# Kernel tuning notes

Hardware: AMD Instinct MI355X
Metric: run time of the kernel (lower is better)

The kernel has to match this reference:

```python
import jax, jax.numpy as jnp
import numpy as np


def _conv1d(x, w, pad):
    # torch F.conv1d is cross-correlation; so is lax.conv_general_dilated.
    # x: (k, c_in, N), w: (c_out, c_in, K) -> (k, c_out, N + 2*pad - K + 1)
    return jax.lax.conv_general_dilated(
        x, w, window_strides=(1,), padding=[(pad, pad)],
        dimension_numbers=("NCH", "OIH", "NCH"))


def setup_inputs() -> dict:
    key = jax.random.key(0)
    k1, k2, k3, k4, k5 = jax.random.split(key, 5)
    k_b, c_out, c_in, N, m = 4, 64, 8, 4096, 8
    z_real = jax.random.normal(k1, (k_b, c_in, N), dtype=jnp.float32)
    z_imag = jax.random.normal(k2, (k_b, c_in, N), dtype=jnp.float32)
    A = jax.random.uniform(k3, (c_out, c_in, 1), jnp.float32, 0.75, 1.25)
    beta = jax.random.uniform(k4, (c_out, c_in, 1), jnp.float32, -np.pi, np.pi)
    bias = jax.random.uniform(k5, (c_out, 1), jnp.float32, -0.1, 0.1)
    return {"z_real": z_real, "z_imag": z_imag, "A": A, "beta": beta,
            "bias": bias, "m": m}


def reference(z_real, z_imag, A, beta, bias, m):
    k_b, c_in, N = z_real.shape
    am = abs(int(m))
    ker = N // (2 * am)  # self.ker_size

    # Complex harmonic kernel: |A| * exp(i*(beta + 2*pi*m*phi/N))
    phi = jnp.arange(ker, dtype=jnp.float32)
    ang = beta + (2.0 * jnp.pi * m / N) * phi  # (c_out, c_in, ker)
    absA = jnp.abs(A)
    wr = absA * jnp.cos(ang)
    wi = absA * jnp.sin(ang)

    # Complex conv via 4 real convs: (zr + i zi) * (wr + i wi)
    rr = _conv1d(z_real, wr, ker)
    ii = _conv1d(z_imag, wi, ker)
    ri = _conv1d(z_real, wi, ker)
    ir = _conv1d(z_imag, wr, ker)
    zraw_r = rr - ii  # (k, c_out, N + ker + 1)
    zraw_i = ri + ir

    # Aliasing fold: gather shifted copies, mask out-of-range, alternate sign.
    n = jnp.arange(-2 * am + 1, 2 * am + 1, dtype=jnp.int32)  # (4|m|,)
    mu = jnp.arange(N, dtype=jnp.int32)[:, None]              # (N, 1)
    ind = mu + ker * n                                        # (N, 4|m|)
    cond = ((ind > 0) & (ind < N + ker)).astype(jnp.float32)
    ind = jnp.clip(ind, 0, N + ker)
    menos_1 = (-1.0) ** (1.0 + n.astype(jnp.float32))         # alternating sign
    sign = cond * menos_1                                     # (N, 4|m|)

    gr = zraw_r[:, :, ind]  # (k, c_out, N, 4|m|)
    gi = zraw_i[:, :, ind]
    sr = jnp.einsum("kcnm,nm->kcn", gr, sign)
    si = jnp.einsum("kcnm,nm->kcn", gi, sign)

    # activation: sigmoid(|z| + bias) * z / (|z| + 1e-5)
    mag = jnp.sqrt(sr * sr + si * si)
    gate = jax.nn.sigmoid(mag + bias) / (mag + 1e-5)
    return gate * sr, gate * si
```

## Files before the change

kernel.cpp:

```cpp
#include <hip/hip_runtime.h>
#include <math.h>


#define KB   4
#define COUT 64
#define CIN  8
#define NN   4096
#define INV_N (1.0f / 4096.0f)
#define INV_2PI 0.15915494309189535f

__global__ void f_reduce_kernel(const float* __restrict__ zr,
                                const float* __restrict__ zi,
                                const int* __restrict__ m_ptr,
                                float* __restrict__ F) {
    const int pair = blockIdx.x;
    const int tid  = threadIdx.x;
    const int m    = *m_ptr;
    const float4* xr = (const float4*)(zr + pair * NN);
    const float4* xi = (const float4*)(zi + pair * NN);

    float fcr = 0.f, fsr = 0.f, fci = 0.f, fsi = 0.f;
    #pragma unroll
    for (int it = 0; it < NN / 1024; ++it) {
        int vidx = it * 256 + tid;
        float4 vr = xr[vidx];
        float4 vi = xi[vidx];
        int t0 = vidx * 4;
        #pragma unroll
        for (int j = 0; j < 4; ++j) {
            int r = (m * (t0 + j)) & (NN - 1);
            float rev = (float)r * INV_N;
            float s = __builtin_amdgcn_sinf(rev);
            float c = __builtin_amdgcn_cosf(rev);
            float a = (&vr.x)[j], b = (&vi.x)[j];
            fcr += a * c;  fsr += a * s;
            fci += b * c;  fsi += b * s;
        }
    }
    #pragma unroll
    for (int off = 32; off > 0; off >>= 1) {
        fcr += __shfl_down(fcr, off);
        fsr += __shfl_down(fsr, off);
        fci += __shfl_down(fci, off);
        fsi += __shfl_down(fsi, off);
    }
    __shared__ float red[4][4];
    int wave = tid >> 6, lane = tid & 63;
    if (lane == 0) {
        red[wave][0] = fcr; red[wave][1] = fsr;
        red[wave][2] = fci; red[wave][3] = fsi;
    }
    __syncthreads();
    if (tid == 0) {
        F[pair * 4 + 0] = red[0][0] + red[1][0] + red[2][0] + red[3][0];
        F[pair * 4 + 1] = red[0][1] + red[1][1] + red[2][1] + red[3][1];
        F[pair * 4 + 2] = red[0][2] + red[1][2] + red[2][2] + red[3][2];
        F[pair * 4 + 3] = red[0][3] + red[1][3] + red[2][3] + red[3][3];
    }
}

__global__ void out_kernel(const float* __restrict__ A,
                           const float* __restrict__ beta,
                           const float* __restrict__ bias,
                           const int* __restrict__ m_ptr,
                           const float* __restrict__ F,
                           float* __restrict__ out) {
    const int blk = blockIdx.x;
    const int b = blk >> 6, o = blk & (COUT - 1);
    const int m = *m_ptr;

    float Gr = 0.f, Hr = 0.f, Gi = 0.f, Hi = 0.f;
    #pragma unroll
    for (int i = 0; i < CIN; ++i) {
        float a  = fabsf(A[o * CIN + i]);
        float rb = beta[o * CIN + i] * INV_2PI;
        float sb = __builtin_amdgcn_sinf(rb);
        float cb = __builtin_amdgcn_cosf(rb);
        float P = a * cb, Q = a * sb;
        const float* f = F + (b * CIN + i) * 4;
        float Fcr = f[0], Fsr = f[1], Fci = f[2], Fsi = f[3];
        Gr += -P * Fcr + Q * Fsr + Q * Fci + P * Fsi;
        Hr += -P * Fsr - Q * Fcr + Q * Fsi - P * Fci;
        Gi += -Q * Fcr - P * Fsr - P * Fci + Q * Fsi;
        Hi +=  P * Fcr - Q * Fsr - Q * Fci - P * Fsi;
    }
    const float bo = bias[o];
    const int base = blk << 12;
    const int half = KB * COUT * NN;

    #pragma unroll
    for (int k = 0; k < NN / 256; ++k) {
        int mu = threadIdx.x + k * 256;
        int r = (m * mu) & (NN - 1);
        float rev = (float)r * INV_N;
        float smu = __builtin_amdgcn_sinf(rev);
        float cmu = __builtin_amdgcn_cosf(rev);
        float sr = -(cmu * Gr + smu * Hr);
        float si = -(cmu * Gi + smu * Hi);
        float mag = sqrtf(sr * sr + si * si);
        float gate = 1.0f / (1.0f + __expf(-(mag + bo))) / (mag + 1e-5f);
        out[base + mu]        = gate * sr;
        out[half + base + mu] = gate * si;
    }
}

extern "C" void kernel_launch(void* const* d_in, const int* in_sizes, int n_in,
                              void* d_out, int out_size, void* d_ws, size_t ws_size,
                              hipStream_t stream) {
    const float* z_real = (const float*)d_in[0];
    const float* z_imag = (const float*)d_in[1];
    const float* A      = (const float*)d_in[2];
    const float* beta   = (const float*)d_in[3];
    const float* bias   = (const float*)d_in[4];
    const int*   m_ptr  = (const int*)d_in[5];
    float* out = (float*)d_out;
    float* F   = (float*)d_ws;

    f_reduce_kernel<<<KB * CIN, 256, 0, stream>>>(z_real, z_imag, m_ptr, F);
    out_kernel<<<KB * COUT, 256, 0, stream>>>(A, beta, bias, m_ptr, F, out);
}
```

Measured before the change: 71.17 us.

## Fuse Fourier reduction and output into one kernel per (batch, out-channel)

Merges the two kernels into a single launch. Each block now recomputes the channel-weighted projection of the input against the m-th harmonic directly, then uses the reduced pair to produce its output row. The output stores are vectorised to float4 and the imaginary part is derived from the same two sums. This removes the second launch and the workspace round trip. In exchange each block re-reads the full 8-channel input for its batch, 64 times redundantly overall, and does more trig and FMA work.

Measured after the change: 77.98 us. +9.6%, slower.

```diff
diff --git a/kernel.cpp b/kernel.cpp
--- a/kernel.cpp
+++ b/kernel.cpp
@@ -6,101 +6,101 @@
 #define COUT 64
 #define CIN  8
 #define NN   4096
-#define INV_N (1.0f / 4096.0f)
+#define INV_N   (1.0f / 4096.0f)
 #define INV_2PI 0.15915494309189535f
 
-__global__ void f_reduce_kernel(const float* __restrict__ zr,
-                                const float* __restrict__ zi,
-                                const int* __restrict__ m_ptr,
-                                float* __restrict__ F) {
-    const int pair = blockIdx.x;
-    const int tid  = threadIdx.x;
-    const int m    = *m_ptr;
-    const float4* xr = (const float4*)(zr + pair * NN);
-    const float4* xi = (const float4*)(zi + pair * NN);
+__global__ __launch_bounds__(256) void capa_fused_kernel(
+    const float* __restrict__ zr,
+    const float* __restrict__ zi,
+    const float* __restrict__ A,
+    const float* __restrict__ beta,
+    const float* __restrict__ bias,
+    const int*   __restrict__ m_ptr,
+    float* __restrict__ out) {
 
-    float fcr = 0.f, fsr = 0.f, fci = 0.f, fsi = 0.f;
+    const int blk = blockIdx.x;
+    const int b = blk >> 6, o = blk & (COUT - 1);
+    const int m = *m_ptr;
+    const int tid = threadIdx.x;
+
+    float P[CIN], Q[CIN];
     #pragma unroll
-    for (int it = 0; it < NN / 1024; ++it) {
-        int vidx = it * 256 + tid;
-        float4 vr = xr[vidx];
-        float4 vi = xi[vidx];
+    for (int i = 0; i < CIN; ++i) {
+        float a  = fabsf(A[o * CIN + i]);
+        float rb = beta[o * CIN + i] * INV_2PI;
+        P[i] = a * __builtin_amdgcn_cosf(rb);
+        Q[i] = a * __builtin_amdgcn_sinf(rb);
+    }
+
+    const float4* xr = (const float4*)(zr + b * CIN * NN);
+    const float4* xi = (const float4*)(zi + b * CIN * NN);
+
+    float gr = 0.f, hr = 0.f;
+    #pragma unroll
+    for (int k = 0; k < NN / 4 / 256; ++k) {
+        int vidx = tid + k * 256;
+        float4 vr[CIN], vi[CIN];
+        #pragma unroll
+        for (int i = 0; i < CIN; ++i) {
+            vr[i] = xr[i * (NN / 4) + vidx];
+            vi[i] = xi[i * (NN / 4) + vidx];
+        }
         int t0 = vidx * 4;
         #pragma unroll
         for (int j = 0; j < 4; ++j) {
+            float X = 0.f, Y = 0.f;
+            #pragma unroll
+            for (int i = 0; i < CIN; ++i) {
+                float a = (&vr[i].x)[j];
+                float c2 = (&vi[i].x)[j];
+                X += -P[i] * a + Q[i] * c2;
+                Y +=  Q[i] * a + P[i] * c2;
+            }
             int r = (m * (t0 + j)) & (NN - 1);
             float rev = (float)r * INV_N;
             float s = __builtin_amdgcn_sinf(rev);
             float c = __builtin_amdgcn_cosf(rev);
-            float a = (&vr.x)[j], b = (&vi.x)[j];
-            fcr += a * c;  fsr += a * s;
-            fci += b * c;  fsi += b * s;
+            gr += c * X + s * Y;
+            hr += s * X - c * Y;
         }
     }
+
     #pragma unroll
     for (int off = 32; off > 0; off >>= 1) {
-        fcr += __shfl_down(fcr, off);
-        fsr += __shfl_down(fsr, off);
-        fci += __shfl_down(fci, off);
-        fsi += __shfl_down(fsi, off);
+        gr += __shfl_down(gr, off);
+        hr += __shfl_down(hr, off);
     }
-    __shared__ float red[4][4];
+    __shared__ float red[4][2];
     int wave = tid >> 6, lane = tid & 63;
-    if (lane == 0) {
-        red[wave][0] = fcr; red[wave][1] = fsr;
-        red[wave][2] = fci; red[wave][3] = fsi;
-    }
+    if (lane == 0) { red[wave][0] = gr; red[wave][1] = hr; }
     __syncthreads();
-    if (tid == 0) {
-        F[pair * 4 + 0] = red[0][0] + red[1][0] + red[2][0] + red[3][0];
-        F[pair * 4 + 1] = red[0][1] + red[1][1] + red[2][1] + red[3][1];
-        F[pair * 4 + 2] = red[0][2] + red[1][2] + red[2][2] + red[3][2];
-        F[pair * 4 + 3] = red[0][3] + red[1][3] + red[2][3] + red[3][3];
-    }
-}
+    const float Gr = red[0][0] + red[1][0] + red[2][0] + red[3][0];
+    const float Hr = red[0][1] + red[1][1] + red[2][1] + red[3][1];
 
-__global__ void out_kernel(const float* __restrict__ A,
-                           const float* __restrict__ beta,
-                           const float* __restrict__ bias,
-                           const int* __restrict__ m_ptr,
-                           const float* __restrict__ F,
-                           float* __restrict__ out) {
-    const int blk = blockIdx.x;
-    const int b = blk >> 6, o = blk & (COUT - 1);
-    const int m = *m_ptr;
-
-    float Gr = 0.f, Hr = 0.f, Gi = 0.f, Hi = 0.f;
-    #pragma unroll
-    for (int i = 0; i < CIN; ++i) {
-        float a  = fabsf(A[o * CIN + i]);
-        float rb = beta[o * CIN + i] * INV_2PI;
-        float sb = __builtin_amdgcn_sinf(rb);
-        float cb = __builtin_amdgcn_cosf(rb);
-        float P = a * cb, Q = a * sb;
-        const float* f = F + (b * CIN + i) * 4;
-        float Fcr = f[0], Fsr = f[1], Fci = f[2], Fsi = f[3];
-        Gr += -P * Fcr + Q * Fsr + Q * Fci + P * Fsi;
-        Hr += -P * Fsr - Q * Fcr + Q * Fsi - P * Fci;
-        Gi += -Q * Fcr - P * Fsr - P * Fci + Q * Fsi;
-        Hi +=  P * Fcr - Q * Fsr - Q * Fci - P * Fsi;
-    }
     const float bo = bias[o];
-    const int base = blk << 12;
-    const int half = KB * COUT * NN;
+    float4* out_r = (float4*)(out + ((long)blk << 12));
+    float4* out_i = (float4*)(out + (long)KB * COUT * NN + ((long)blk << 12));
 
     #pragma unroll
-    for (int k = 0; k < NN / 256; ++k) {
-        int mu = threadIdx.x + k * 256;
-        int r = (m * mu) & (NN - 1);
-        float rev = (float)r * INV_N;
-        float smu = __builtin_amdgcn_sinf(rev);
-        float cmu = __builtin_amdgcn_cosf(rev);
-        float sr = -(cmu * Gr + smu * Hr);
-        float si = -(cmu * Gi + smu * Hi);
-        float mag = sqrtf(sr * sr + si * si);
-        float gate = 1.0f / (1.0f + __expf(-(mag + bo))) / (mag + 1e-5f);
-        out[base + mu]        = gate * sr;
-        out[half + base + mu] = gate * si;
+    for (int k = 0; k < NN / 4 / 256; ++k) {
+        int vidx = tid + k * 256;
+        int mu0 = vidx * 4;
+        float4 o1, o2;
+        #pragma unroll
+        for (int j = 0; j < 4; ++j) {
+            int r = (m * (mu0 + j)) & (NN - 1);
+            float rev = (float)r * INV_N;
+            float s = __builtin_amdgcn_sinf(rev);
+            float c = __builtin_amdgcn_cosf(rev);
+            float sr = -(c * Gr + s * Hr);
+            float si = s * Gr - c * Hr;
+            float mag = sqrtf(sr * sr + si * si);
+            float gate = 1.0f / ((1.0f + __expf(-(mag + bo))) * (mag + 1e-5f));
+            (&o1.x)[j] = gate * sr;
+            (&o2.x)[j] = gate * si;
+        }
+        out_r[vidx] = o1;
+        out_i[vidx] = o2;
     }
 }
 
@@ -114,8 +114,7 @@
     const float* bias   = (const float*)d_in[4];
     const int*   m_ptr  = (const int*)d_in[5];
     float* out = (float*)d_out;
-    float* F   = (float*)d_ws;
 
-    f_reduce_kernel<<<KB * CIN, 256, 0, stream>>>(z_real, z_imag, m_ptr, F);
-    out_kernel<<<KB * COUT, 256, 0, stream>>>(A, beta, bias, m_ptr, F, out);
+    capa_fused_kernel<<<KB * COUT, 256, 0, stream>>>(
+        z_real, z_imag, A, beta, bias, m_ptr, out);
 }
```
